# Kernel optimization log

Hardware: AMD Instinct MI355X
Metric: run time of the kernel (lower is better)

The kernel has to match this reference:

```python
import jax, jax.numpy as jnp
import numpy as np

N_NODES = 50000
N_EDGES = 800000
IN_FEAT = 256
OUT_FEAT = 256
NUM_RELS = 64
NUM_BASES = 8


def setup_inputs() -> dict:
    key = jax.random.key(0)
    ks = jax.random.split(key, 9)
    x = jax.random.normal(ks[0], (N_NODES, IN_FEAT), dtype=jnp.float32)
    src = jax.random.randint(ks[1], (N_EDGES,), 0, N_NODES, dtype=jnp.int32)
    dst = jax.random.randint(ks[2], (N_EDGES,), 0, N_NODES, dtype=jnp.int32)
    etypes = jax.random.randint(ks[3], (N_EDGES,), 0, NUM_RELS, dtype=jnp.int32)
    norm = jax.random.uniform(ks[4], (N_EDGES, 1), dtype=jnp.float32)
    # glorot-style params
    s_w = (6.0 / (IN_FEAT + OUT_FEAT)) ** 0.5
    weight = jax.random.uniform(ks[5], (NUM_BASES, IN_FEAT, OUT_FEAT), jnp.float32, -s_w, s_w)
    s_c = (6.0 / (NUM_RELS + NUM_BASES)) ** 0.5
    w_comp = jax.random.uniform(ks[6], (NUM_RELS, NUM_BASES), jnp.float32, -s_c, s_c)
    h_bias = jnp.zeros((OUT_FEAT,), jnp.float32)
    loop_weight = jax.random.uniform(ks[7], (IN_FEAT, OUT_FEAT), jnp.float32, -s_w, s_w)
    return {"x": x, "src": src, "dst": dst, "etypes": etypes, "norm": norm,
            "weight": weight, "w_comp": w_comp, "h_bias": h_bias,
            "loop_weight": loop_weight}


def reference(x, src, dst, etypes, norm, weight, w_comp, h_bias, loop_weight):
    # Basis regularizer with num_bases < num_rels:
    #   W_r = sum_b w_comp[r, b] * V_b
    # Per-edge message: msg_e = (x[src_e] @ W_{etype_e}) * norm_e,
    # aggregated by sum onto destination nodes. Since the map is linear,
    # we aggregate per basis first, then apply V_b (8 dense GEMMs).
    n_nodes = x.shape[0]
    coef = w_comp[etypes]                      # [E, B] per-edge basis coeffs
    xs = x[src] * norm                         # [E, D] normalized source feats
    out = jnp.zeros((n_nodes, weight.shape[2]), x.dtype)
    for b in range(weight.shape[0]):           # small fixed loop over bases
        agg = jax.ops.segment_sum(xs * coef[:, b:b + 1], dst,
                                  num_segments=n_nodes)   # [N, D]
        out = out + agg @ weight[b]            # [N, O]
    out = out + h_bias + x @ loop_weight       # bias + self-loop
    return jax.nn.relu(out)
```

## Files before the change

### kernel.cpp

```cpp
#include <hip/hip_runtime.h>
#include <hip/hip_bf16.h>
#include <stdint.h>

#define N_NODES 50000
#define N_EDGES 800000
#define IN_FEAT 256
#define OUT_FEAT 256
#define NUM_RELS 64
#define NUM_BASES 8
#define KTOT 2304
#define KAGG 2048
#define MP 50048
#define SCAN_BLKS 196

typedef __attribute__((ext_vector_type(8))) __bf16 bf16x8;
typedef __attribute__((ext_vector_type(4))) __bf16 bf16x4;
typedef __attribute__((ext_vector_type(4))) float f32x4;
typedef __attribute__((ext_vector_type(2))) float f32x2;

static __device__ __forceinline__ void gload_lds16(const void* g, void* l) {
  auto gp = (const __attribute__((address_space(1))) void*)(uintptr_t)g;
  auto lp = (__attribute__((address_space(3))) void*)(uint32_t)(uintptr_t)l;
  __builtin_amdgcn_global_load_lds(gp, lp, 16, 0, 0);
}

__global__ void k_prex(const float* __restrict__ x, __bf16* __restrict__ xb) {
  int i = blockIdx.x * 256 + threadIdx.x;
  const float4* xp = (const float4*)x;
  float4 u = xp[i * 2], v = xp[i * 2 + 1];
  bf16x8 o;
  o[0] = (__bf16)u.x; o[1] = (__bf16)u.y; o[2] = (__bf16)u.z; o[3] = (__bf16)u.w;
  o[4] = (__bf16)v.x; o[5] = (__bf16)v.y; o[6] = (__bf16)v.z; o[7] = (__bf16)v.w;
  *(bf16x8*)(xb + (size_t)i * 8) = o;
}

__global__ void k_count(const int* __restrict__ dst, int* __restrict__ deg) {
  int e = blockIdx.x * 256 + threadIdx.x;
  atomicAdd(&deg[dst[e]], 1);
}

__global__ void k_scan1(const int* __restrict__ deg, int* __restrict__ offs,
                        int* __restrict__ bsum) {
  __shared__ int s[256];
  int t = threadIdx.x;
  int i = blockIdx.x * 256 + t;
  int v = (i < N_NODES) ? deg[i] : 0;
  s[t] = v;
  __syncthreads();
  for (int d = 1; d < 256; d <<= 1) {
    int y = (t >= d) ? s[t - d] : 0;
    __syncthreads();
    s[t] += y;
    __syncthreads();
  }
  if (i < N_NODES) offs[i] = s[t] - v;
  if (t == 255) bsum[blockIdx.x] = s[255];
}

__global__ void k_scan2(const int* __restrict__ bsum, int* __restrict__ bbase) {
  __shared__ int s[256];
  int t = threadIdx.x;
  int v = (t < SCAN_BLKS) ? bsum[t] : 0;
  s[t] = v;
  __syncthreads();
  for (int d = 1; d < 256; d <<= 1) {
    int y = (t >= d) ? s[t - d] : 0;
    __syncthreads();
    s[t] += y;
    __syncthreads();
  }
  if (t < SCAN_BLKS) bbase[t] = s[t] - v;
}

__global__ void k_scan3(int* __restrict__ offs, const int* __restrict__ bbase,
                        int* __restrict__ fill) {
  int i = blockIdx.x * 256 + threadIdx.x;
  if (i < N_NODES) {
    int o = offs[i] + bbase[blockIdx.x];
    offs[i] = o;
    fill[i] = o;
  }
}

__global__ void k_scatter(const int* __restrict__ dst, const int* __restrict__ srcv,
                          const int* __restrict__ ety, const float* __restrict__ norm,
                          int* __restrict__ fill, uint2* __restrict__ erec) {
  int e = blockIdx.x * 256 + threadIdx.x;
  int pos = atomicAdd(&fill[dst[e]], 1);
  erec[pos] = make_uint2((unsigned)srcv[e] | ((unsigned)ety[e] << 16),
                         __float_as_uint(norm[e]));
}

__global__ __launch_bounds__(256) void k_agg(
    const __bf16* __restrict__ xb, const float* __restrict__ w_comp,
    const int* __restrict__ offs, const int* __restrict__ fin,
    const uint2* __restrict__ erec, __bf16* __restrict__ A) {
  __shared__ float wc[NUM_RELS * NUM_BASES];
  int t = threadIdx.x;
  wc[t] = w_comp[t];
  wc[t + 256] = w_comp[t + 256];
  __syncthreads();

  int wid = t >> 6, lane = t & 63;
  int node = blockIdx.x * 4 + wid;

  f32x2 acc[NUM_BASES][2];
#pragma unroll
  for (int b = 0; b < NUM_BASES; ++b) {
    acc[b][0] = f32x2{0.f, 0.f};
    acc[b][1] = f32x2{0.f, 0.f};
  }

  int i0 = offs[node];
  int cnt = fin[node] - i0;
  const uint2* rp = erec + i0;
  int lo4 = lane * 4;

  int i = 0;
  for (; i + 4 <= cnt; i += 4) {
    uint2 r[4];
#pragma unroll
    for (int j = 0; j < 4; ++j) r[j] = rp[i + j];
    uint2 xv[4];
#pragma unroll
    for (int j = 0; j < 4; ++j) {
      int sv = r[j].x & 0xffff;
      xv[j] = *(const uint2*)(xb + (size_t)sv * IN_FEAT + lo4);
    }
#pragma unroll
    for (int j = 0; j < 4; ++j) {
      int et = r[j].x >> 16;
      float nm = __uint_as_float(r[j].y);
      float a0 = __uint_as_float(xv[j].x << 16);
      float a1 = __uint_as_float(xv[j].x & 0xffff0000u);
      float a2 = __uint_as_float(xv[j].y << 16);
      float a3 = __uint_as_float(xv[j].y & 0xffff0000u);
      f32x2 v0 = {a0 * nm, a1 * nm};
      f32x2 v1 = {a2 * nm, a3 * nm};
      f32x4 cl = *(const f32x4*)&wc[et * 8];
      f32x4 ch = *(const f32x4*)&wc[et * 8 + 4];
#pragma unroll
      for (int b = 0; b < 4; ++b) {
        acc[b][0] += v0 * cl[b];
        acc[b][1] += v1 * cl[b];
        acc[b + 4][0] += v0 * ch[b];
        acc[b + 4][1] += v1 * ch[b];
      }
    }
  }
  for (; i < cnt; ++i) {
    uint2 r = rp[i];
    int sv = r.x & 0xffff;
    int et = r.x >> 16;
    float nm = __uint_as_float(r.y);
    uint2 xv = *(const uint2*)(xb + (size_t)sv * IN_FEAT + lo4);
    float a0 = __uint_as_float(xv.x << 16);
    float a1 = __uint_as_float(xv.x & 0xffff0000u);
    float a2 = __uint_as_float(xv.y << 16);
    float a3 = __uint_as_float(xv.y & 0xffff0000u);
    f32x2 v0 = {a0 * nm, a1 * nm};
    f32x2 v1 = {a2 * nm, a3 * nm};
    f32x4 cl = *(const f32x4*)&wc[et * 8];
    f32x4 ch = *(const f32x4*)&wc[et * 8 + 4];
#pragma unroll
    for (int b = 0; b < 4; ++b) {
      acc[b][0] += v0 * cl[b];
      acc[b][1] += v1 * cl[b];
      acc[b + 4][0] += v0 * ch[b];
      acc[b + 4][1] += v1 * ch[b];
    }
  }

  __bf16* Ar = A + (size_t)node * KAGG + lo4;
#pragma unroll
  for (int b = 0; b < NUM_BASES; ++b) {
    bf16x4 o;
    o[0] = (__bf16)acc[b][0][0];
    o[1] = (__bf16)acc[b][0][1];
    o[2] = (__bf16)acc[b][1][0];
    o[3] = (__bf16)acc[b][1][1];
    *(bf16x4*)(Ar + b * 256) = o;
  }
}

__global__ void k_prepw(const float* __restrict__ weight, const float* __restrict__ loop_w,
                        __bf16* __restrict__ Wt) {
  int o = blockIdx.x;
  int t = threadIdx.x;
#pragma unroll
  for (int c = 0; c < 9; ++c) {
    int r = c * 256 + t;
    float v = (r < 2048) ? weight[(size_t)r * 256 + o]
                         : loop_w[(size_t)(r - 2048) * 256 + o];
    Wt[(size_t)o * KTOT + r] = (__bf16)v;
  }
}

__global__ __launch_bounds__(256, 2) void k_gemm(const __bf16* __restrict__ A,
                                                 const __bf16* __restrict__ xb,
                                                 const __bf16* __restrict__ Wt,
                                                 const float* __restrict__ bias,
                                                 float* __restrict__ out) {
  __shared__ __align__(16) __bf16 sA[64 * 32];
  __shared__ __align__(16) __bf16 sB[256 * 32];

  int t = threadIdx.x;
  int wid = t >> 6, lane = t & 63;
  int tm = blockIdx.x;
  int rfw = __builtin_amdgcn_readfirstlane(wid);

  f32x4 acc[4][4];
#pragma unroll
  for (int m = 0; m < 4; ++m)
#pragma unroll
    for (int n = 0; n < 4; ++n) acc[m][n] = f32x4{0.f, 0.f, 0.f, 0.f};

  int frow = lane & 15;
  int fkb = (lane >> 4) * 16;

  for (int kt = 0; kt < 72; ++kt) {
    int k0 = kt * 32;
    int arow = tm * 64 + (t >> 2);
    const __bf16* ga = (kt < 64)
        ? A + (size_t)arow * KAGG + k0 + (t & 3) * 8
        : xb + (size_t)arow * IN_FEAT + (k0 - KAGG) + (t & 3) * 8;
    gload_lds16(ga, (char*)sA + rfw * 1024);
#pragma unroll
    for (int it = 0; it < 4; ++it) {
      int c = it * 256 + t;
      const __bf16* gb = Wt + (size_t)(c >> 2) * KTOT + k0 + (c & 3) * 8;
      gload_lds16(gb, (char*)sB + (it * 256 + rfw * 64) * 16);
    }
    __syncthreads();

    bf16x8 af[4], bfr[4];
#pragma unroll
    for (int m = 0; m < 4; ++m)
      af[m] = *(const bf16x8*)((const char*)sA + (m * 16 + frow) * 64 + fkb);
#pragma unroll
    for (int n = 0; n < 4; ++n)
      bfr[n] = *(const bf16x8*)((const char*)sB + (wid * 64 + n * 16 + frow) * 64 + fkb);
#pragma unroll
    for (int m = 0; m < 4; ++m)
#pragma unroll
      for (int n = 0; n < 4; ++n)
        acc[m][n] = __builtin_amdgcn_mfma_f32_16x16x32_bf16(af[m], bfr[n], acc[m][n], 0, 0, 0);
    __syncthreads();
  }

  int r0 = (lane >> 4) * 4;
  int c0 = lane & 15;
#pragma unroll
  for (int m = 0; m < 4; ++m) {
    int rowb = tm * 64 + m * 16 + r0;
#pragma unroll
    for (int n = 0; n < 4; ++n) {
      int col = wid * 64 + n * 16 + c0;
      float bv = bias[col];
#pragma unroll
      for (int r = 0; r < 4; ++r) {
        int row = rowb + r;
        if (row < N_NODES) {
          float v = acc[m][n][r] + bv;
          out[(size_t)row * OUT_FEAT + col] = v > 0.f ? v : 0.f;
        }
      }
    }
  }
}

extern "C" void kernel_launch(void* const* d_in, const int* in_sizes, int n_in,
                              void* d_out, int out_size, void* d_ws, size_t ws_size,
                              hipStream_t stream) {
  const float* x      = (const float*)d_in[0];
  const int*   src    = (const int*)d_in[1];
  const int*   dst    = (const int*)d_in[2];
  const int*   ety    = (const int*)d_in[3];
  const float* norm   = (const float*)d_in[4];
  const float* weight = (const float*)d_in[5];
  const float* w_comp = (const float*)d_in[6];
  const float* h_bias = (const float*)d_in[7];
  const float* loop_w = (const float*)d_in[8];
  float* out = (float*)d_out;

  char* ws = (char*)d_ws;
  __bf16* A  = (__bf16*)ws;
  size_t off = (size_t)MP * KAGG * 2;
  __bf16* xb = (__bf16*)(ws + off);
  off += (size_t)MP * IN_FEAT * 2;
  __bf16* Wt = (__bf16*)(ws + off);
  off += (size_t)256 * KTOT * 2;
  uint2* erec = (uint2*)(ws + off);
  off += (size_t)N_EDGES * 8;
  int* deg   = (int*)(ws + off);
  int* offs  = deg + N_NODES;
  int* fill  = offs + N_NODES;
  int* bsum  = fill + N_NODES;
  int* bbase = bsum + 256;

  hipMemsetAsync(deg, 0, N_NODES * sizeof(int), stream);
  k_prex<<<(N_NODES * IN_FEAT / 8) / 256, 256, 0, stream>>>(x, xb);
  k_count<<<N_EDGES / 256, 256, 0, stream>>>(dst, deg);
  k_scan1<<<SCAN_BLKS, 256, 0, stream>>>(deg, offs, bsum);
  k_scan2<<<1, 256, 0, stream>>>(bsum, bbase);
  k_scan3<<<SCAN_BLKS, 256, 0, stream>>>(offs, bbase, fill);
  k_scatter<<<N_EDGES / 256, 256, 0, stream>>>(dst, src, ety, norm, fill, erec);
  k_agg<<<N_NODES / 4, 256, 0, stream>>>(xb, w_comp, offs, fill, erec, A);
  k_prepw<<<256, 256, 0, stream>>>(weight, loop_w, Wt);
  k_gemm<<<MP / 64, 256, 0, stream>>>(A, xb, Wt, h_bias, out);
}
```

Baseline: 342.3 us.

## Enlarge GEMM tile with LDS swizzle, split agg edges across waves, fuse scans

The GEMM now computes 128x256 output tiles with a 2x2 wave layout, which halves how often the weight matrix is reloaded. It precomputes the global pointers and XOR-swizzles the LDS k-chunks to avoid bank conflicts. The aggregation kernel assigns two waves per node, each handling half the edges, and combines the partial sums through shared memory; this adds parallelism and memory-level concurrency for the gathers. The scan2 and scan3 kernels are merged so each block reduces the preceding block sums itself, which removes one launch. The costs are more registers in the GEMM (32 accumulator tiles per wave) and an extra LDS exchange in the aggregation.

After: 554.6 us. 62.0% more time.

```diff
diff --git a/kernel.cpp b/kernel.cpp
--- a/kernel.cpp
+++ b/kernel.cpp
@@ -57,26 +57,20 @@
   if (t == 255) bsum[blockIdx.x] = s[255];
 }
 
-__global__ void k_scan2(const int* __restrict__ bsum, int* __restrict__ bbase) {
+__global__ void k_scan3(int* __restrict__ offs, const int* __restrict__ bsum,
+                        int* __restrict__ fill) {
   __shared__ int s[256];
   int t = threadIdx.x;
-  int v = (t < SCAN_BLKS) ? bsum[t] : 0;
-  s[t] = v;
+  s[t] = (t < SCAN_BLKS && t < blockIdx.x) ? bsum[t] : 0;
   __syncthreads();
-  for (int d = 1; d < 256; d <<= 1) {
-    int y = (t >= d) ? s[t - d] : 0;
+  for (int d = 128; d; d >>= 1) {
+    if (t < d) s[t] += s[t + d];
     __syncthreads();
-    s[t] += y;
-    __syncthreads();
-  }
-  if (t < SCAN_BLKS) bbase[t] = s[t] - v;
-}
-
-__global__ void k_scan3(int* __restrict__ offs, const int* __restrict__ bbase,
-                        int* __restrict__ fill) {
-  int i = blockIdx.x * 256 + threadIdx.x;
+  }
+  int base = s[0];
+  int i = blockIdx.x * 256 + t;
   if (i < N_NODES) {
-    int o = offs[i] + bbase[blockIdx.x];
+    int o = offs[i] + base;
     offs[i] = o;
     fill[i] = o;
   }
@@ -96,13 +90,15 @@
     const int* __restrict__ offs, const int* __restrict__ fin,
     const uint2* __restrict__ erec, __bf16* __restrict__ A) {
   __shared__ float wc[NUM_RELS * NUM_BASES];
+  __shared__ float sx[4 * 64 * 17];
   int t = threadIdx.x;
   wc[t] = w_comp[t];
   wc[t + 256] = w_comp[t + 256];
   __syncthreads();
 
   int wid = t >> 6, lane = t & 63;
-  int node = blockIdx.x * 4 + wid;
+  int p = wid >> 1, h = wid & 1;
+  int node = blockIdx.x * 2 + p;
 
   f32x2 acc[NUM_BASES][2];
 #pragma unroll
@@ -113,30 +109,28 @@
 
   int i0 = offs[node];
   int cnt = fin[node] - i0;
-  const uint2* rp = erec + i0;
+  int c0 = (cnt + 1) >> 1;
+  int myn = h ? (cnt - c0) : c0;
+  const uint2* rp = erec + i0 + h * c0;
   int lo4 = lane * 4;
 
   int i = 0;
-  for (; i + 4 <= cnt; i += 4) {
+  for (; i + 4 <= myn; i += 4) {
     uint2 r[4];
 #pragma unroll
     for (int j = 0; j < 4; ++j) r[j] = rp[i + j];
     uint2 xv[4];
 #pragma unroll
-    for (int j = 0; j < 4; ++j) {
-      int sv = r[j].x & 0xffff;
-      xv[j] = *(const uint2*)(xb + (size_t)sv * IN_FEAT + lo4);
-    }
+    for (int j = 0; j < 4; ++j)
+      xv[j] = *(const uint2*)(xb + (size_t)(r[j].x & 0xffff) * IN_FEAT + lo4);
 #pragma unroll
     for (int j = 0; j < 4; ++j) {
       int et = r[j].x >> 16;
       float nm = __uint_as_float(r[j].y);
-      float a0 = __uint_as_float(xv[j].x << 16);
-      float a1 = __uint_as_float(xv[j].x & 0xffff0000u);
-      float a2 = __uint_as_float(xv[j].y << 16);
-      float a3 = __uint_as_float(xv[j].y & 0xffff0000u);
-      f32x2 v0 = {a0 * nm, a1 * nm};
-      f32x2 v1 = {a2 * nm, a3 * nm};
+      f32x2 v0 = {__uint_as_float(xv[j].x << 16) * nm,
+                  __uint_as_float(xv[j].x & 0xffff0000u) * nm};
+      f32x2 v1 = {__uint_as_float(xv[j].y << 16) * nm,
+                  __uint_as_float(xv[j].y & 0xffff0000u) * nm};
       f32x4 cl = *(const f32x4*)&wc[et * 8];
       f32x4 ch = *(const f32x4*)&wc[et * 8 + 4];
 #pragma unroll
@@ -148,18 +142,15 @@
       }
     }
   }
-  for (; i < cnt; ++i) {
+  for (; i < myn; ++i) {
     uint2 r = rp[i];
-    int sv = r.x & 0xffff;
     int et = r.x >> 16;
     float nm = __uint_as_float(r.y);
-    uint2 xv = *(const uint2*)(xb + (size_t)sv * IN_FEAT + lo4);
-    float a0 = __uint_as_float(xv.x << 16);
-    float a1 = __uint_as_float(xv.x & 0xffff0000u);
-    float a2 = __uint_as_float(xv.y << 16);
-    float a3 = __uint_as_float(xv.y & 0xffff0000u);
-    f32x2 v0 = {a0 * nm, a1 * nm};
-    f32x2 v1 = {a2 * nm, a3 * nm};
+    uint2 xv = *(const uint2*)(xb + (size_t)(r.x & 0xffff) * IN_FEAT + lo4);
+    f32x2 v0 = {__uint_as_float(xv.x << 16) * nm,
+                __uint_as_float(xv.x & 0xffff0000u) * nm};
+    f32x2 v1 = {__uint_as_float(xv.y << 16) * nm,
+                __uint_as_float(xv.y & 0xffff0000u) * nm};
     f32x4 cl = *(const f32x4*)&wc[et * 8];
     f32x4 ch = *(const f32x4*)&wc[et * 8 + 4];
 #pragma unroll
@@ -171,15 +162,27 @@
     }
   }
 
+  float* slot = &sx[(size_t)wid * 64 * 17 + lane * 17];
+  int og = (1 - h) * 4;
+#pragma unroll
+  for (int b = 0; b < 4; ++b) {
+    slot[b * 4 + 0] = acc[og + b][0][0];
+    slot[b * 4 + 1] = acc[og + b][0][1];
+    slot[b * 4 + 2] = acc[og + b][1][0];
+    slot[b * 4 + 3] = acc[og + b][1][1];
+  }
+  __syncthreads();
+  const float* ps = &sx[(size_t)(wid ^ 1) * 64 * 17 + lane * 17];
+  int mg = h * 4;
   __bf16* Ar = A + (size_t)node * KAGG + lo4;
 #pragma unroll
-  for (int b = 0; b < NUM_BASES; ++b) {
+  for (int b = 0; b < 4; ++b) {
     bf16x4 o;
-    o[0] = (__bf16)acc[b][0][0];
-    o[1] = (__bf16)acc[b][0][1];
-    o[2] = (__bf16)acc[b][1][0];
-    o[3] = (__bf16)acc[b][1][1];
-    *(bf16x4*)(Ar + b * 256) = o;
+    o[0] = (__bf16)(acc[mg + b][0][0] + ps[b * 4 + 0]);
+    o[1] = (__bf16)(acc[mg + b][0][1] + ps[b * 4 + 1]);
+    o[2] = (__bf16)(acc[mg + b][1][0] + ps[b * 4 + 2]);
+    o[3] = (__bf16)(acc[mg + b][1][1] + ps[b * 4 + 3]);
+    *(bf16x4*)(Ar + (mg + b) * 256) = o;
   }
 }
 
@@ -201,61 +204,83 @@
                                                  const __bf16* __restrict__ Wt,
                                                  const float* __restrict__ bias,
                                                  float* __restrict__ out) {
-  __shared__ __align__(16) __bf16 sA[64 * 32];
+  __shared__ __align__(16) __bf16 sA[128 * 32];
   __shared__ __align__(16) __bf16 sB[256 * 32];
 
   int t = threadIdx.x;
   int wid = t >> 6, lane = t & 63;
   int tm = blockIdx.x;
+  int wr = wid >> 1, wc = wid & 1;
   int rfw = __builtin_amdgcn_readfirstlane(wid);
 
-  f32x4 acc[4][4];
+  f32x4 acc[4][8];
 #pragma unroll
   for (int m = 0; m < 4; ++m)
 #pragma unroll
-    for (int n = 0; n < 4; ++n) acc[m][n] = f32x4{0.f, 0.f, 0.f, 0.f};
+    for (int n = 0; n < 8; ++n) acc[m][n] = f32x4{0.f, 0.f, 0.f, 0.f};
 
   int frow = lane & 15;
-  int fkb = (lane >> 4) * 16;
-
-  for (int kt = 0; kt < 72; ++kt) {
+  int kb = (((lane >> 4) ^ ((frow >> 1) & 3)) << 4);
+
+  const __bf16* gaP[2];
+  const __bf16* gxP[2];
+#pragma unroll
+  for (int it = 0; it < 2; ++it) {
+    int L = it * 256 + t;
+    int row = L >> 2;
+    int q = (L & 3) ^ ((row >> 1) & 3);
+    gaP[it] = A + (size_t)(tm * 128 + row) * KAGG + q * 8;
+    gxP[it] = xb + (size_t)(tm * 128 + row) * IN_FEAT + q * 8;
+  }
+  const __bf16* gbP[4];
+#pragma unroll
+  for (int it = 0; it < 4; ++it) {
+    int L = it * 256 + t;
+    int row = L >> 2;
+    int q = (L & 3) ^ ((row >> 1) & 3);
+    gbP[it] = Wt + (size_t)row * KTOT + q * 8;
+  }
+
+#define KSTEP(A0, A1, K0)                                                   \
+  do {                                                                      \
+    gload_lds16((A0), (char*)sA + rfw * 1024);                              \
+    gload_lds16((A1), (char*)sA + 4096 + rfw * 1024);                       \
+    _Pragma("unroll") for (int it = 0; it < 4; ++it)                        \
+        gload_lds16(gbP[it] + (K0), (char*)sB + (it * 256 + rfw * 64) * 16);\
+    __syncthreads();                                                        \
+    bf16x8 af[4], bfr[8];                                                   \
+    _Pragma("unroll") for (int m = 0; m < 4; ++m)                           \
+        af[m] = *(const bf16x8*)((const char*)sA +                          \
+                                 (wr * 64 + m * 16 + frow) * 64 + kb);      \
+    _Pragma("unroll") for (int n = 0; n < 8; ++n)                           \
+        bfr[n] = *(const bf16x8*)((const char*)sB +                         \
+                                  (wc * 128 + n * 16 + frow) * 64 + kb);    \
+    _Pragma("unroll") for (int m = 0; m < 4; ++m)                           \
+        _Pragma("unroll") for (int n = 0; n < 8; ++n)                       \
+            acc[m][n] = __builtin_amdgcn_mfma_f32_16x16x32_bf16(            \
+                af[m], bfr[n], acc[m][n], 0, 0, 0);                         \
+    __syncthreads();                                                        \
+  } while (0)
+
+  for (int kt = 0; kt < 64; ++kt) {
     int k0 = kt * 32;
-    int arow = tm * 64 + (t >> 2);
-    const __bf16* ga = (kt < 64)
-        ? A + (size_t)arow * KAGG + k0 + (t & 3) * 8
-        : xb + (size_t)arow * IN_FEAT + (k0 - KAGG) + (t & 3) * 8;
-    gload_lds16(ga, (char*)sA + rfw * 1024);
-#pragma unroll
-    for (int it = 0; it < 4; ++it) {
-      int c = it * 256 + t;
-      const __bf16* gb = Wt + (size_t)(c >> 2) * KTOT + k0 + (c & 3) * 8;
-      gload_lds16(gb, (char*)sB + (it * 256 + rfw * 64) * 16);
-    }
-    __syncthreads();
-
-    bf16x8 af[4], bfr[4];
-#pragma unroll
-    for (int m = 0; m < 4; ++m)
-      af[m] = *(const bf16x8*)((const char*)sA + (m * 16 + frow) * 64 + fkb);
-#pragma unroll
-    for (int n = 0; n < 4; ++n)
-      bfr[n] = *(const bf16x8*)((const char*)sB + (wid * 64 + n * 16 + frow) * 64 + fkb);
-#pragma unroll
-    for (int m = 0; m < 4; ++m)
-#pragma unroll
-      for (int n = 0; n < 4; ++n)
-        acc[m][n] = __builtin_amdgcn_mfma_f32_16x16x32_bf16(af[m], bfr[n], acc[m][n], 0, 0, 0);
-    __syncthreads();
-  }
+    KSTEP(gaP[0] + k0, gaP[1] + k0, k0);
+  }
+  for (int kt = 64; kt < 72; ++kt) {
+    int k0 = kt * 32;
+    int kx = k0 - KAGG;
+    KSTEP(gxP[0] + kx, gxP[1] + kx, k0);
+  }
+#undef KSTEP
 
   int r0 = (lane >> 4) * 4;
   int c0 = lane & 15;
 #pragma unroll
   for (int m = 0; m < 4; ++m) {
-    int rowb = tm * 64 + m * 16 + r0;
-#pragma unroll
-    for (int n = 0; n < 4; ++n) {
-      int col = wid * 64 + n * 16 + c0;
+    int rowb = tm * 128 + wr * 64 + m * 16 + r0;
+#pragma unroll
+    for (int n = 0; n < 8; ++n) {
+      int col = wc * 128 + n * 16 + c0;
       float bv = bias[col];
 #pragma unroll
       for (int r = 0; r < 4; ++r) {
@@ -296,16 +321,14 @@
   int* offs  = deg + N_NODES;
   int* fill  = offs + N_NODES;
   int* bsum  = fill + N_NODES;
-  int* bbase = bsum + 256;
 
   hipMemsetAsync(deg, 0, N_NODES * sizeof(int), stream);
   k_prex<<<(N_NODES * IN_FEAT / 8) / 256, 256, 0, stream>>>(x, xb);
   k_count<<<N_EDGES / 256, 256, 0, stream>>>(dst, deg);
   k_scan1<<<SCAN_BLKS, 256, 0, stream>>>(deg, offs, bsum);
-  k_scan2<<<1, 256, 0, stream>>>(bsum, bbase);
-  k_scan3<<<SCAN_BLKS, 256, 0, stream>>>(offs, bbase, fill);
+  k_scan3<<<SCAN_BLKS, 256, 0, stream>>>(offs, bsum, fill);
   k_scatter<<<N_EDGES / 256, 256, 0, stream>>>(dst, src, ety, norm, fill, erec);
-  k_agg<<<N_NODES / 4, 256, 0, stream>>>(xb, w_comp, offs, fill, erec, A);
+  k_agg<<<N_NODES / 2, 256, 0, stream>>>(xb, w_comp, offs, fill, erec, A);
   k_prepw<<<256, 256, 0, stream>>>(weight, loop_w, Wt);
-  k_gemm<<<MP / 64, 256, 0, stream>>>(A, xb, Wt, h_bias, out);
-}
+  k_gemm<<<MP / 128, 256, 0, stream>>>(A, xb, Wt, h_bias, out);
+}
```
